# Optimization experiments

Measured on AMD Instinct MI355X. Metric: run time of the kernel, lower is better.

The kernel has to match this reference:

```python
import jax, jax.numpy as jnp
import numpy as np
import math

B, L, D, H, MAX_K = 8, 4096, 2048, 16, 1024
HD = D // H


def setup_inputs() -> dict:
    key = jax.random.key(0)
    ks = jax.random.split(key, 20)
    x = jax.random.normal(ks[0], (B, L, D), dtype=jnp.float32)
    register = jax.random.normal(ks[1], (B, D), dtype=jnp.float32)
    # mask with exactly MAX_K True per row -> max_k == MAX_K, no ragged padding
    perms = jax.vmap(lambda k: jax.random.permutation(k, L))(jax.random.split(ks[2], B))
    sel = perms[:, :MAX_K]
    mask = jnp.zeros((B, L), dtype=bool).at[jnp.arange(B)[:, None], sel].set(True)
    s = 1.0 / math.sqrt(D)
    def lin(k):
        k1, k2 = jax.random.split(k)
        return (jax.random.uniform(k1, (D, D), jnp.float32, -s, s),
                jax.random.uniform(k2, (D,), jnp.float32, -s, s))
    Wq, bq = lin(ks[3]); Wk, bk = lin(ks[4]); Wv, bv = lin(ks[5])
    Wrk, brk = lin(ks[6]); Wrv, brv = lin(ks[7]); Wo, bo = lin(ks[8])
    return {"x": x, "mask": mask, "register": register,
            "Wq": Wq, "bq": bq, "Wk": Wk, "bk": bk, "Wv": Wv, "bv": bv,
            "Wrk": Wrk, "brk": brk, "Wrv": Wrv, "brv": brv, "Wo": Wo, "bo": bo}


def reference(x, mask, register, Wq, bq, Wk, bk, Wv, bv, Wrk, brk, Wrv, brv, Wo, bo):
    Bb, Ll, Dd = x.shape
    scale = math.sqrt(HD)
    # stable argsort puts True(=selected) tokens first, in ascending position order
    idx = jnp.argsort(jnp.logical_not(mask), axis=1, stable=True)[:, :MAX_K]  # [B,K]
    pos = idx
    sig = jnp.take_along_axis(x, idx[:, :, None], axis=1)  # [B,K,D]
    Q = (sig @ Wq.T + bq).reshape(Bb, MAX_K, H, HD)
    Kt = (sig @ Wk.T + bk)
    Vt = (sig @ Wv.T + bv)
    Kr = (register @ Wrk.T + brk)[:, None, :]  # [B,1,D]
    Vr = (register @ Wrv.T + brv)[:, None, :]
    Kall = jnp.concatenate([Kt, Kr], axis=1).reshape(Bb, MAX_K + 1, H, HD)
    Vall = jnp.concatenate([Vt, Vr], axis=1).reshape(Bb, MAX_K + 1, H, HD)
    scores = jnp.einsum('bqhd,bkhd->bhqk', Q, Kall) / scale  # [B,H,K,K+1]
    causal = jnp.where(pos[:, :, None] < pos[:, None, :], -1e9, 0.0)  # [B,K,K]
    full_mask = jnp.concatenate([causal, jnp.zeros((Bb, MAX_K, 1), x.dtype)], axis=2)[:, None]
    attn = jax.nn.softmax(scores + full_mask, axis=-1)
    out = jnp.einsum('bhqk,bkhd->bqhd', attn, Vall).reshape(Bb, MAX_K, Dd)
    y = out @ Wo.T + bo
    res = x.at[jnp.arange(Bb)[:, None], idx].set(y)
    return res
```

## Files before the change

kernel.cpp:

```cpp
#include <hip/hip_runtime.h>
#include <hip/hip_bf16.h>

#define B_  8
#define L_  4096
#define D_  2048
#define H_  16
#define HD_ 128
#define MK_ 1024
#define VTP 1040

typedef __attribute__((ext_vector_type(8))) short short8;
typedef __attribute__((ext_vector_type(4))) float f32x4;

__device__ inline unsigned short f2bf(float f) {
  unsigned int u = __float_as_uint(f);
  unsigned int r = (u + 0x7fffu + ((u >> 16) & 1u)) >> 16;
  return (unsigned short)r;
}

__device__ __forceinline__ void gload_lds16(const void* g, void* l) {
  __builtin_amdgcn_global_load_lds(
      (const __attribute__((address_space(1))) void*)g,
      (__attribute__((address_space(3))) void*)l, 16, 0, 0);
}

__global__ __launch_bounds__(256) void prep1_kernel(
    const void* __restrict__ maskv, int* __restrict__ rowmap,
    const float* __restrict__ W0, const float* __restrict__ W1,
    const float* __restrict__ W2, const float* __restrict__ W3,
    unsigned short* __restrict__ Wb) {
  int bid = blockIdx.x;
  int tid = threadIdx.x;
  if (bid < 8) {
    __shared__ int cnt;
    __shared__ int cnts[256];
    const unsigned char* m8 = (const unsigned char*)maskv;
    if (tid == 0) cnt = 0;
    __syncthreads();
    int local = 0;
    for (int i = tid; i < B_ * L_; i += 256) local += (m8[i] != 0);
    atomicAdd(&cnt, local);
    __syncthreads();
    int cv = cnt;
    int t = 0;
    if (cv == B_ * MK_)      t = 0;
    else if (cv == 2 * MK_)  t = 1;
    else if (cv == 4 * MK_)  t = 2;
    int b = bid;
    unsigned char loc[16];
    int c = 0;
    for (int j = 0; j < 16; ++j) {
      int pos = tid * 16 + j;
      int mv;
      if (t == 1)      mv = ((const int*)maskv)[b * L_ + pos] != 0;
      else if (t == 2) mv = ((const float*)maskv)[b * L_ + pos] != 0.0f;
      else             mv = m8[b * L_ + pos] != 0;
      loc[j] = (unsigned char)mv; c += mv;
    }
    cnts[tid] = c;
    __syncthreads();
    for (int off = 1; off < 256; off <<= 1) {
      int v = (tid >= off) ? cnts[tid - off] : 0;
      __syncthreads();
      cnts[tid] += v;
      __syncthreads();
    }
    int rank = cnts[tid] - c;
    for (int j = 0; j < 16; ++j) {
      if (loc[j]) {
        if (rank < MK_) rowmap[b * MK_ + rank] = b * L_ + tid * 16 + j;
        ++rank;
      }
    }
  } else {
    const size_t per = (size_t)D_ * D_;
    int cb = bid - 8;
    int slab = cb >> 11;
    const float* W = (slab == 0) ? W0 : (slab == 1) ? W1 : (slab == 2) ? W2 : W3;
    size_t i = ((size_t)(cb & 2047) * 256 + tid) * 8;
    float4 a = *(const float4*)(W + i);
    float4 b4 = *(const float4*)(W + i + 4);
    uint4 o;
    o.x = f2bf(a.x)  | ((unsigned)f2bf(a.y)  << 16);
    o.y = f2bf(a.z)  | ((unsigned)f2bf(a.w)  << 16);
    o.z = f2bf(b4.x) | ((unsigned)f2bf(b4.y) << 16);
    o.w = f2bf(b4.z) | ((unsigned)f2bf(b4.w) << 16);
    *(uint4*)(Wb + slab * per + i) = o;
  }
}

__global__ __launch_bounds__(256) void prep2_kernel(
    const float* __restrict__ x, const int* __restrict__ rowmap,
    unsigned short* __restrict__ sig,
    const float* __restrict__ reg, const float* __restrict__ Wrk, const float* __restrict__ brk,
    const float* __restrict__ Wrv, const float* __restrict__ brv,
    unsigned short* __restrict__ Kb, unsigned short* __restrict__ Vt) {
  int bid = blockIdx.x;
  int tid = threadIdx.x;
  if (bid < 8192) {
    int row = bid;
    const float* src = x + (size_t)rowmap[row] * D_;
    unsigned short* dst = sig + (size_t)row * D_;
    float4 a = ((const float4*)src)[tid * 2];
    float4 b4 = ((const float4*)src)[tid * 2 + 1];
    uint4 o;
    o.x = f2bf(a.x)  | ((unsigned)f2bf(a.y)  << 16);
    o.y = f2bf(a.z)  | ((unsigned)f2bf(a.w)  << 16);
    o.z = f2bf(b4.x) | ((unsigned)f2bf(b4.y) << 16);
    o.w = f2bf(b4.z) | ((unsigned)f2bf(b4.w) << 16);
    *(uint4*)(dst + tid * 8) = o;
  } else {
    int gw = ((bid - 8192) * 256 + tid) >> 6;
    int lane = tid & 63;
    int mat = gw >> 11;
    int n = gw & 2047;
    const float* W = mat ? Wrv : Wrk;
    const float* wrow = W + (size_t)n * D_;
    float s[8] = {};
    for (int j = 0; j < 8; ++j) {
      int e = j * 256 + lane * 4;
      float4 wv = *(const float4*)(wrow + e);
#pragma unroll
      for (int b = 0; b < 8; ++b) {
        float4 rv = *(const float4*)(reg + (size_t)b * D_ + e);
        s[b] += wv.x * rv.x + wv.y * rv.y + wv.z * rv.z + wv.w * rv.w;
      }
    }
#pragma unroll
    for (int off = 32; off; off >>= 1)
#pragma unroll
      for (int b = 0; b < 8; ++b) s[b] += __shfl_down(s[b], off);
    if (lane == 0) {
      float bias = (mat ? brv : brk)[n];
#pragma unroll
      for (int b = 0; b < 8; ++b) {
        unsigned short v = f2bf(s[b] + bias);
        if (mat) {
          Vt[(((size_t)b * 16 + (n >> 7)) * 128 + (n & 127)) * VTP + 1024] = v;
        } else {
          Kb[((size_t)b * 1025 + 1024) * D_ + n] = v;
        }
      }
    }
  }
}

template<int FUSED>
__global__ __launch_bounds__(512, 2) void gemm8_kernel(
    const unsigned short* __restrict__ A, const unsigned short* __restrict__ Bw,
    const float* __restrict__ b0, const float* __restrict__ b1, const float* __restrict__ b2,
    void* __restrict__ O0, void* __restrict__ O1, void* __restrict__ O2,
    const int* __restrict__ rowmap, float qalpha, int nbt, int matfix) {
  __shared__ __align__(16) unsigned short lds[2][2][16384];
  int tid = threadIdx.x, lane = tid & 63, w = tid >> 6;
  int g = lane >> 4, l15 = lane & 15;
  int wm = w >> 2, wn = w & 3;

  int bid = blockIdx.x;
  int xcd = bid & 7, j = bid >> 3;
  int mb = xcd * 4 + j / nbt, nb = j % nbt;
  int m0 = mb * 256, n0 = nb * 256;

  f32x4 acc[2][4][4] = {};

  size_t aoff[4], boff[4];
  int ldsoff[4];
#pragma unroll
  for (int i = 0; i < 4; ++i) {
    int chunk = tid + i * 512;
    int row = chunk >> 3;
    int gslot = (chunk & 7) ^ (row & 7);
    aoff[i] = (size_t)(m0 + row) * D_ + gslot * 8;
    boff[i] = (size_t)(n0 + row) * D_ + gslot * 8;
    ldsoff[i] = (w * 64 + i * 512) * 8;
  }

#define STAGE_A(kt, BUF) {                                              \
    _Pragma("unroll")                                                   \
    for (int i_ = 0; i_ < 4; ++i_)                                      \
      gload_lds16(A + aoff[i_] + (kt) * 64, &lds[BUF][0][ldsoff[i_]]);  \
  }
#define STAGE_B(kt, BUF) {                                              \
    _Pragma("unroll")                                                   \
    for (int i_ = 0; i_ < 4; ++i_)                                      \
      gload_lds16(Bw + boff[i_] + (kt) * 64, &lds[BUF][1][ldsoff[i_]]); \
  }
#define RD_A(dst, BUF, h, kk) {                                         \
    _Pragma("unroll")                                                   \
    for (int mf_ = 0; mf_ < 4; ++mf_) {                                 \
      int r_ = wm * 128 + (h) * 64 + mf_ * 16 + l15;                    \
      dst[mf_] = *(const short8*)(&lds[BUF][0][r_ * 64 + (((kk) * 4 + g) ^ (r_ & 7)) * 8]); } \
  }
#define RD_B(dst, BUF, kk) {                                            \
    _Pragma("unroll")                                                   \
    for (int nf_ = 0; nf_ < 4; ++nf_) {                                 \
      int r_ = wn * 64 + nf_ * 16 + l15;                                \
      dst[nf_] = *(const short8*)(&lds[BUF][1][r_ * 64 + (((kk) * 4 + g) ^ (r_ & 7)) * 8]); } \
  }
#define MFMA16(h, af, bf) {                                             \
    _Pragma("unroll")                                                   \
    for (int mf_ = 0; mf_ < 4; ++mf_)                                   \
      _Pragma("unroll")                                                 \
      for (int nf_ = 0; nf_ < 4; ++nf_)                                 \
        acc[h][mf_][nf_] = __builtin_amdgcn_mfma_f32_16x16x32_bf16(af[mf_], bf[nf_], acc[h][mf_][nf_], 0, 0, 0); \
  }

  STAGE_A(0, 0); STAGE_B(0, 0);
  asm volatile("s_waitcnt vmcnt(0)" ::: "memory");
  __builtin_amdgcn_s_barrier();

  short8 afE[4], afO[4], bf0[4], bf1[4];

#define KTILE(kt, BUF)                                                    \
  {                                                                       \
    RD_B(bf0, BUF, 0); RD_B(bf1, BUF, 1); RD_A(afE, BUF, 0, 0);           \
     \
    RD_A(afO, BUF, 0, 1);                                                 \
    if ((kt) + 1 < 32) { STAGE_A((kt) + 1, BUF ^ 1); STAGE_B((kt) + 1, BUF ^ 1); } \
    asm volatile("s_waitcnt lgkmcnt(4)" ::: "memory");                    \
    __builtin_amdgcn_sched_barrier(0);                                    \
    __builtin_amdgcn_s_setprio(1);                                        \
    MFMA16(0, afE, bf0);                                                  \
    __builtin_amdgcn_s_setprio(0);                                        \
                                                       \
    RD_A(afE, BUF, 1, 0);                                                 \
    asm volatile("s_waitcnt lgkmcnt(4)" ::: "memory");                    \
    __builtin_amdgcn_sched_barrier(0);                                    \
    __builtin_amdgcn_s_setprio(1);                                        \
    MFMA16(0, afO, bf1);                                                  \
    __builtin_amdgcn_s_setprio(0);                                        \
                                                       \
    RD_A(afO, BUF, 1, 1);                                                 \
    asm volatile("s_waitcnt lgkmcnt(4)" ::: "memory");                    \
    __builtin_amdgcn_sched_barrier(0);                                    \
    __builtin_amdgcn_s_setprio(1);                                        \
    MFMA16(1, afE, bf0);                                                  \
    __builtin_amdgcn_s_setprio(0);                                        \
                                                       \
    asm volatile("s_waitcnt lgkmcnt(0)" ::: "memory");                    \
    __builtin_amdgcn_sched_barrier(0);                                    \
    __builtin_amdgcn_s_setprio(1);                                        \
    MFMA16(1, afO, bf1);                                                  \
    __builtin_amdgcn_s_setprio(0);                                        \
    asm volatile("s_waitcnt vmcnt(0)" ::: "memory");                      \
    __builtin_amdgcn_s_barrier();                                         \
  }

  for (int kt2 = 0; kt2 < 16; ++kt2) {
    KTILE(2 * kt2,     0);
    KTILE(2 * kt2 + 1, 1);
  }
#undef KTILE
#undef MFMA16
#undef RD_A
#undef RD_B
#undef STAGE_A
#undef STAGE_B

  int mat = 0;
  const float* bias = b0;
  float alpha = 1.0f;
  int n0l = n0;
  if (FUSED) {
    mat = (matfix >= 0) ? matfix : (n0 >> 11);
    bias = (mat == 0) ? b0 : ((mat == 1) ? b1 : b2);
    alpha = (mat == 0) ? qalpha : 1.0f;
    n0l = n0 & 2047;
  }

#pragma unroll
  for (int ph = 0; ph < 2; ++ph) {
#pragma unroll
    for (int mf = 0; mf < 4; ++mf) {
#pragma unroll
      for (int nf = 0; nf < 4; ++nf) {
        int nn = n0l + wn * 64 + nf * 16 + l15;
        float bvv = bias[nn];
        int m = m0 + wm * 128 + ph * 64 + mf * 16 + g * 4;
        if (FUSED) {
          if (mat == 2) {
            int bb = m >> 10, tok = m & 1023;
            size_t base = (((size_t)bb * 16 + (nn >> 7)) * 128 + (nn & 127)) * VTP + tok;
            uint2 u;
            u.x = f2bf(acc[ph][mf][nf][0] + bvv) | ((unsigned)f2bf(acc[ph][mf][nf][1] + bvv) << 16);
            u.y = f2bf(acc[ph][mf][nf][2] + bvv) | ((unsigned)f2bf(acc[ph][mf][nf][3] + bvv) << 16);
            *(uint2*)((unsigned short*)O2 + base) = u;
          } else {
            unsigned short* out = (mat == 0) ? (unsigned short*)O0 : (unsigned short*)O1;
#pragma unroll
            for (int r = 0; r < 4; ++r) {
              float v = (acc[ph][mf][nf][r] + bvv) * alpha;
              int mm = m + r;
              int row = (mat == 1) ? mm + (mm >> 10) : mm;
              out[(size_t)row * D_ + nn] = f2bf(v);
            }
          }
        } else {
#pragma unroll
          for (int r = 0; r < 4; ++r) {
            int row = rowmap[m + r];
            ((float*)O0)[(size_t)row * D_ + nn] = acc[ph][mf][nf][r] + bvv;
          }
        }
      }
    }
  }
}

__device__ __forceinline__ void stage_k(const unsigned short* Kbase, unsigned short* dst,
                                        int kv0, int w, int lane) {
#pragma unroll
  for (int i = 0; i < 2; ++i) {
    int ib = w * 2 + i;
    int row = ib * 4 + (lane >> 4);
    int sl = (lane & 15) ^ (row & 7);
    int krow = kv0 + row; if (krow > MK_) krow = MK_;
    gload_lds16(Kbase + (size_t)krow * D_ + sl * 8, dst + ib * 512);
  }
}
__device__ __forceinline__ void stage_v(const unsigned short* Vbase, unsigned short* dst,
                                        int kv0, int w, int lane) {
#pragma unroll
  for (int i = 0; i < 2; ++i) {
    int ib = w * 2 + i;
    int row = ib * 8 + (lane >> 3);
    int sl = (lane & 7) ^ (row & 7);
    gload_lds16(Vbase + (size_t)row * VTP + kv0 + sl * 8, dst + ib * 512);
  }
}

#define NF4 16777216

__global__ __launch_bounds__(512) void attn_kernel(
    const unsigned short* __restrict__ Qb, const unsigned short* __restrict__ Kb,
    const unsigned short* __restrict__ Vt, unsigned short* __restrict__ Ob,
    const float4* __restrict__ xsrc, float4* __restrict__ xdst) {
  int bx = blockIdx.x;
  int gq = bx >> 7;
  int qi = 7 - gq;
  int bh = bx & 127;
  int b = bh >> 4, h = bh & 15;
  int tid = threadIdx.x, lane = tid & 63, w = tid >> 6;
  int g = lane >> 4, l15 = lane & 15;
  int q0 = qi * 128;
  int nt = 2 * qi + 3;

  size_t cpyBase = ((size_t)128 * (18 * gq - gq * gq) + (size_t)(bx & 127) * nt) * 2048;

  __shared__ __align__(16) unsigned short Ks[64 * 128];
  __shared__ __align__(16) unsigned short Vts[128 * 64];
  __shared__ __align__(16) unsigned short Ps[8][16][72];

  const unsigned short* Kbase = Kb + (size_t)b * 1025 * D_ + h * HD_;
  const unsigned short* Vbase = Vt + (size_t)bh * 128 * VTP;

  short8 qf[4];
  {
    const unsigned short* qrow = Qb + (size_t)(b * MK_ + q0 + w * 16 + l15) * D_ + h * HD_;
#pragma unroll
    for (int kk = 0; kk < 4; ++kk) qf[kk] = *(const short8*)(qrow + kk * 32 + g * 8);
  }

  f32x4 oacc[8] = {};
  float mrow[4], lrow[4];
#pragma unroll
  for (int r = 0; r < 4; ++r) { mrow[r] = -__builtin_inff(); lrow[r] = 0.f; }

  int qminw = q0 + w * 16;

  stage_k(Kbase, Ks, 0, w, lane);

  for (int t = 0; t < nt; ++t) {
    int kv0 = (t < nt - 1) ? t * 64 : MK_;

    size_t ci[4];
    float4 cv[4];
    {
      size_t i0 = cpyBase + (size_t)t * 2048 + tid;
#pragma unroll
      for (int jj = 0; jj < 4; ++jj) {
        size_t ix = i0 + jj * 512;
        ci[jj] = ix < NF4 ? ix : (NF4 - 1);
        cv[jj] = xsrc[ci[jj]];
      }
    }

    stage_v(Vbase, Vts, kv0, w, lane);
    if (t == 0) asm volatile("s_waitcnt vmcnt(6)" ::: "memory");
    else        asm volatile("s_waitcnt vmcnt(10)" ::: "memory");
    __builtin_amdgcn_s_barrier();

    bool active = (t == nt - 1) || (t * 64 <= qminw + 15);
    f32x4 sacc[4] = {};
    if (active) {
      __builtin_amdgcn_s_setprio(1);
#pragma unroll
      for (int kk = 0; kk < 4; ++kk) {
#pragma unroll
        for (int nf = 0; nf < 4; ++nf) {
          int krow = nf * 16 + l15;
          int sw = (kk * 4 + g) ^ (krow & 7);
          short8 kf = *(const short8*)(Ks + krow * 128 + sw * 8);
          sacc[nf] = __builtin_amdgcn_mfma_f32_16x16x32_bf16(qf[kk], kf, sacc[nf], 0, 0, 0);
        }
      }
      __builtin_amdgcn_s_setprio(0);
    }

    __builtin_amdgcn_s_barrier();
    if (t + 1 < nt) {
      int kv1 = (t + 1 < nt - 1) ? (t + 1) * 64 : MK_;
      stage_k(Kbase, Ks, kv1, w, lane);
    }

    if (active) {
      if (t == nt - 1) {
#pragma unroll
        for (int nf = 0; nf < 4; ++nf) {
          int col = nf * 16 + l15;
          if (col != 0) {
#pragma unroll
            for (int r = 0; r < 4; ++r) sacc[nf][r] = -1e9f;
          }
        }
      } else if (t * 64 + 63 > qminw) {
        int qb = qminw - t * 64 + g * 4;
#pragma unroll
        for (int nf = 0; nf < 4; ++nf) {
          int col = nf * 16 + l15;
#pragma unroll
          for (int r = 0; r < 4; ++r)
            if (col > qb + r) sacc[nf][r] = -1e9f;
        }
      }

      float pm[4]; bool need = false;
#pragma unroll
      for (int r = 0; r < 4; ++r) {
        float mx = fmaxf(fmaxf(sacc[0][r], sacc[1][r]), fmaxf(sacc[2][r], sacc[3][r]));
        mx = fmaxf(mx, __shfl_xor(mx, 1));
        mx = fmaxf(mx, __shfl_xor(mx, 2));
        mx = fmaxf(mx, __shfl_xor(mx, 4));
        mx = fmaxf(mx, __shfl_xor(mx, 8));
        pm[r] = mx;
        need |= (mx > mrow[r] + 8.0f);
      }
      if (__any((int)need)) {
#pragma unroll
        for (int r = 0; r < 4; ++r) {
          float mnew = fmaxf(mrow[r], pm[r]);
          float sf = exp2f(mrow[r] - mnew);
          mrow[r] = mnew;
          lrow[r] *= sf;
#pragma unroll
          for (int i = 0; i < 8; ++i) oacc[i][r] *= sf;
        }
      }
      float rs[4] = {0.f, 0.f, 0.f, 0.f};
#pragma unroll
      for (int nf = 0; nf < 4; ++nf) {
#pragma unroll
        for (int r = 0; r < 4; ++r) {
          float p = exp2f(sacc[nf][r] - mrow[r]);
          sacc[nf][r] = p;
          rs[r] += p;
        }
      }
#pragma unroll
      for (int r = 0; r < 4; ++r) {
        float s = rs[r];
        s += __shfl_xor(s, 1);
        s += __shfl_xor(s, 2);
        s += __shfl_xor(s, 4);
        s += __shfl_xor(s, 8);
        lrow[r] += s;
      }
#pragma unroll
      for (int nf = 0; nf < 4; ++nf)
#pragma unroll
        for (int r = 0; r < 4; ++r)
          Ps[w][g * 4 + r][nf * 16 + l15] = f2bf(sacc[nf][r]);
    }

    if (t + 1 < nt) asm volatile("s_waitcnt vmcnt(2)" ::: "memory");
    else            asm volatile("s_waitcnt vmcnt(0)" ::: "memory");

#pragma unroll
    for (int jj = 0; jj < 4; ++jj) xdst[ci[jj]] = cv[jj];

    __builtin_amdgcn_s_barrier();

    if (active) {
      __builtin_amdgcn_s_setprio(1);
#pragma unroll
      for (int kk = 0; kk < 2; ++kk) {
        short8 pf = *(const short8*)(&Ps[w][l15][kk * 32 + g * 8]);
#pragma unroll
        for (int nf = 0; nf < 8; ++nf) {
          int vrow = nf * 16 + l15;
          int sw = (kk * 4 + g) ^ (vrow & 7);
          short8 vf = *(const short8*)(Vts + vrow * 64 + sw * 8);
          oacc[nf] = __builtin_amdgcn_mfma_f32_16x16x32_bf16(pf, vf, oacc[nf], 0, 0, 0);
        }
      }
      __builtin_amdgcn_s_setprio(0);
    }
    __builtin_amdgcn_s_barrier();
  }

#pragma unroll
  for (int nf = 0; nf < 8; ++nf) {
#pragma unroll
    for (int r = 0; r < 4; ++r) {
      size_t row = (size_t)b * MK_ + q0 + w * 16 + g * 4 + r;
      Ob[row * D_ + h * HD_ + nf * 16 + l15] = f2bf(oacc[nf][r] / lrow[r]);
    }
  }
}

extern "C" void kernel_launch(void* const* d_in, const int* in_sizes, int n_in,
                              void* d_out, int out_size, void* d_ws, size_t ws_size,
                              hipStream_t stream) {
  const float* x    = (const float*)d_in[0];
  const void*  mask = d_in[1];
  const float* reg  = (const float*)d_in[2];
  const float* Wq   = (const float*)d_in[3];
  const float* bq   = (const float*)d_in[4];
  const float* Wk   = (const float*)d_in[5];
  const float* bk   = (const float*)d_in[6];
  const float* Wv   = (const float*)d_in[7];
  const float* bv   = (const float*)d_in[8];
  const float* Wrk  = (const float*)d_in[9];
  const float* brk  = (const float*)d_in[10];
  const float* Wrv  = (const float*)d_in[11];
  const float* brv  = (const float*)d_in[12];
  const float* Wo   = (const float*)d_in[13];
  const float* bo   = (const float*)d_in[14];

  char* ws = (char*)d_ws;
  int* rowmap          = (int*)(ws + 256);
  char* p = ws + 66048;
  unsigned short* sig = (unsigned short*)p;              p += (size_t)8192 * 2048 * 2;
  unsigned short* Qb  = (unsigned short*)p;              p += (size_t)8192 * 2048 * 2;
  unsigned short* Kb  = (unsigned short*)p;              p += (size_t)8200 * 2048 * 2;
  unsigned short* Vtb = (unsigned short*)p;              p += ((size_t)16384 * VTP + 64) * 2;
  unsigned short* Wbf = (unsigned short*)p;
  unsigned short* Ob  = sig;

  const size_t need_fused = (size_t)(p - ws) + (size_t)8192 * 2048 * 2;
  const bool fused = (ws_size >= need_fused);

  const float qalpha = 0.08838834764831845f * 1.4426950408889634f;
  const size_t per = (size_t)2048 * 2048;

  if (fused) {
    prep1_kernel<<<8200, 256, 0, stream>>>(mask, rowmap, Wq, Wk, Wv, Wo, Wbf);
    prep2_kernel<<<9216, 256, 0, stream>>>(x, rowmap, sig, reg, Wrk, brk, Wrv, brv, Kb, Vtb);
    gemm8_kernel<1><<<768, 512, 0, stream>>>(sig, Wbf, bq, bk, bv, Qb, Kb, Vtb,
                                             nullptr, qalpha, 24, -1);
    attn_kernel<<<1024, 512, 0, stream>>>(Qb, Kb, Vtb, Ob, (const float4*)x, (float4*)d_out);
    gemm8_kernel<0><<<256, 512, 0, stream>>>(Ob, Wbf + 3 * per, bo, nullptr, nullptr,
                                             d_out, nullptr, nullptr, rowmap, 1.0f, 8, -1);
  } else {
    prep1_kernel<<<8, 256, 0, stream>>>(mask, rowmap, Wq, Wk, Wv, Wo, Wbf);
    prep2_kernel<<<9216, 256, 0, stream>>>(x, rowmap, sig, reg, Wrk, brk, Wrv, brv, Kb, Vtb);
    prep1_kernel<<<8200, 256, 0, stream>>>(mask, rowmap, Wq, Wq, Wq, Wq, Wbf);
    gemm8_kernel<1><<<256, 512, 0, stream>>>(sig, Wbf, bq, bk, bv, Qb, Kb, Vtb,
                                             nullptr, qalpha, 8, 0);
    prep1_kernel<<<8200, 256, 0, stream>>>(mask, rowmap, Wk, Wk, Wk, Wk, Wbf);
    gemm8_kernel<1><<<256, 512, 0, stream>>>(sig, Wbf, bq, bk, bv, Qb, Kb, Vtb,
                                             nullptr, qalpha, 8, 1);
    prep1_kernel<<<8200, 256, 0, stream>>>(mask, rowmap, Wv, Wv, Wv, Wv, Wbf);
    gemm8_kernel<1><<<256, 512, 0, stream>>>(sig, Wbf, bq, bk, bv, Qb, Kb, Vtb,
                                             nullptr, qalpha, 8, 2);
    attn_kernel<<<1024, 512, 0, stream>>>(Qb, Kb, Vtb, Ob, (const float4*)x, (float4*)d_out);
    prep1_kernel<<<8200, 256, 0, stream>>>(mask, rowmap, Wo, Wo, Wo, Wo, Wbf);
    gemm8_kernel<0><<<256, 512, 0, stream>>>(Ob, Wbf, bo, nullptr, nullptr,
                                             d_out, nullptr, nullptr, rowmap, 1.0f, 8, -1);
  }
}
```

Measured before the change: 513.4 us.

## Split GEMM tiles into half-tile quadrants with fine-grained staged prefetch

Restructures the 256x256 bf16 GEMM main loop so each operand tile is split into two 128-row halves, staged and consumed in four phases per k-step. Each half is prefetched into the other buffer as soon as its current copy has been read, with partial vmcnt waits and barriers between phases. This replaces one coarse wait per k-tile with finer overlap of global-to-LDS loads and MFMA work. Warp-to-output mapping changes to 64x32 subtiles per half, and the epilogue indexing is updated to match. The cost is more barriers per k-step and a more fragile wait-count schedule.

```diff
diff --git a/kernel.cpp b/kernel.cpp
--- a/kernel.cpp
+++ b/kernel.cpp
@@ -148,10 +148,10 @@
 template<int FUSED>
 __global__ __launch_bounds__(512, 2) void gemm8_kernel(
     const unsigned short* __restrict__ A, const unsigned short* __restrict__ Bw,
-    const float* __restrict__ b0, const float* __restrict__ b1, const float* __restrict__ b2,
+    const float* __restrict__ b0v, const float* __restrict__ b1v, const float* __restrict__ b2v,
     void* __restrict__ O0, void* __restrict__ O1, void* __restrict__ O2,
     const int* __restrict__ rowmap, float qalpha, int nbt, int matfix) {
-  __shared__ __align__(16) unsigned short lds[2][2][16384];
+  __shared__ __align__(16) unsigned short lds[2][2][2][8192];
   int tid = threadIdx.x, lane = tid & 63, w = tid >> 6;
   int g = lane >> 4, l15 = lane & 15;
   int wm = w >> 2, wn = w & 3;
@@ -163,133 +163,113 @@
 
   f32x4 acc[2][4][4] = {};
 
-  size_t aoff[4], boff[4];
-  int ldsoff[4];
-#pragma unroll
-  for (int i = 0; i < 4; ++i) {
-    int chunk = tid + i * 512;
-    int row = chunk >> 3;
-    int gslot = (chunk & 7) ^ (row & 7);
-    aoff[i] = (size_t)(m0 + row) * D_ + gslot * 8;
-    boff[i] = (size_t)(n0 + row) * D_ + gslot * 8;
-    ldsoff[i] = (w * 64 + i * 512) * 8;
-  }
-
-#define STAGE_A(kt, BUF) {                                              \
-    _Pragma("unroll")                                                   \
-    for (int i_ = 0; i_ < 4; ++i_)                                      \
-      gload_lds16(A + aoff[i_] + (kt) * 64, &lds[BUF][0][ldsoff[i_]]);  \
-  }
-#define STAGE_B(kt, BUF) {                                              \
-    _Pragma("unroll")                                                   \
-    for (int i_ = 0; i_ < 4; ++i_)                                      \
-      gload_lds16(Bw + boff[i_] + (kt) * 64, &lds[BUF][1][ldsoff[i_]]); \
-  }
-#define RD_A(dst, BUF, h, kk) {                                         \
-    _Pragma("unroll")                                                   \
-    for (int mf_ = 0; mf_ < 4; ++mf_) {                                 \
-      int r_ = wm * 128 + (h) * 64 + mf_ * 16 + l15;                    \
-      dst[mf_] = *(const short8*)(&lds[BUF][0][r_ * 64 + (((kk) * 4 + g) ^ (r_ & 7)) * 8]); } \
-  }
-#define RD_B(dst, BUF, kk) {                                            \
-    _Pragma("unroll")                                                   \
-    for (int nf_ = 0; nf_ < 4; ++nf_) {                                 \
-      int r_ = wn * 64 + nf_ * 16 + l15;                                \
-      dst[nf_] = *(const short8*)(&lds[BUF][1][r_ * 64 + (((kk) * 4 + g) ^ (r_ & 7)) * 8]); } \
-  }
-#define MFMA16(h, af, bf) {                                             \
-    _Pragma("unroll")                                                   \
-    for (int mf_ = 0; mf_ < 4; ++mf_)                                   \
-      _Pragma("unroll")                                                 \
-      for (int nf_ = 0; nf_ < 4; ++nf_)                                 \
-        acc[h][mf_][nf_] = __builtin_amdgcn_mfma_f32_16x16x32_bf16(af[mf_], bf[nf_], acc[h][mf_][nf_], 0, 0, 0); \
-  }
-
-  STAGE_A(0, 0); STAGE_B(0, 0);
-  asm volatile("s_waitcnt vmcnt(0)" ::: "memory");
-  __builtin_amdgcn_s_barrier();
-
-  short8 afE[4], afO[4], bf0[4], bf1[4];
-
-#define KTILE(kt, BUF)                                                    \
-  {                                                                       \
-    RD_B(bf0, BUF, 0); RD_B(bf1, BUF, 1); RD_A(afE, BUF, 0, 0);           \
-     \
-    RD_A(afO, BUF, 0, 1);                                                 \
-    if ((kt) + 1 < 32) { STAGE_A((kt) + 1, BUF ^ 1); STAGE_B((kt) + 1, BUF ^ 1); } \
-    asm volatile("s_waitcnt lgkmcnt(4)" ::: "memory");                    \
-    __builtin_amdgcn_sched_barrier(0);                                    \
-    __builtin_amdgcn_s_setprio(1);                                        \
-    MFMA16(0, afE, bf0);                                                  \
-    __builtin_amdgcn_s_setprio(0);                                        \
-                                                       \
-    RD_A(afE, BUF, 1, 0);                                                 \
-    asm volatile("s_waitcnt lgkmcnt(4)" ::: "memory");                    \
-    __builtin_amdgcn_sched_barrier(0);                                    \
-    __builtin_amdgcn_s_setprio(1);                                        \
-    MFMA16(0, afO, bf1);                                                  \
-    __builtin_amdgcn_s_setprio(0);                                        \
-                                                       \
-    RD_A(afO, BUF, 1, 1);                                                 \
-    asm volatile("s_waitcnt lgkmcnt(4)" ::: "memory");                    \
-    __builtin_amdgcn_sched_barrier(0);                                    \
-    __builtin_amdgcn_s_setprio(1);                                        \
-    MFMA16(1, afE, bf0);                                                  \
-    __builtin_amdgcn_s_setprio(0);                                        \
-                                                       \
-    asm volatile("s_waitcnt lgkmcnt(0)" ::: "memory");                    \
-    __builtin_amdgcn_sched_barrier(0);                                    \
-    __builtin_amdgcn_s_setprio(1);                                        \
-    MFMA16(1, afO, bf1);                                                  \
-    __builtin_amdgcn_s_setprio(0);                                        \
-    asm volatile("s_waitcnt vmcnt(0)" ::: "memory");                      \
-    __builtin_amdgcn_s_barrier();                                         \
-  }
-
-  for (int kt2 = 0; kt2 < 16; ++kt2) {
-    KTILE(2 * kt2,     0);
-    KTILE(2 * kt2 + 1, 1);
-  }
-#undef KTILE
-#undef MFMA16
+  int c0 = tid, c1 = tid + 512;
+  int r0 = c0 >> 3, s0 = (c0 & 7) ^ (r0 & 7);
+  int r1 = c1 >> 3, s1 = (c1 & 7) ^ (r1 & 7);
+  int dst0 = (w * 64) * 8;
+  int dst1 = (w * 64 + 512) * 8;
+
+#define STAGE(MAT, HH, BUF, kt) {                                                 \
+    const unsigned short* sp_ = (MAT) ? Bw : A;                                   \
+    int gb_ = (MAT) ? n0 : m0;                                                    \
+    gload_lds16(sp_ + (size_t)(gb_ + (HH)*128 + r0) * D_ + (kt)*64 + s0*8,        \
+                &lds[BUF][MAT][HH][dst0]);                                        \
+    gload_lds16(sp_ + (size_t)(gb_ + (HH)*128 + r1) * D_ + (kt)*64 + s1*8,        \
+                &lds[BUF][MAT][HH][dst1]);                                        \
+  }
+
+  short8 a_[4][2], bb0[2][2], bb1[2][2];
+#define RD_A(HH, BUF) { _Pragma("unroll")                                         \
+    for (int mf_ = 0; mf_ < 4; ++mf_) {                                           \
+      int rr_ = wm * 64 + mf_ * 16 + l15;                                         \
+      _Pragma("unroll")                                                           \
+      for (int ks_ = 0; ks_ < 2; ++ks_)                                           \
+        a_[mf_][ks_] = *(const short8*)(&lds[BUF][0][HH][rr_ * 64 + ((ks_*4+g)^(rr_&7))*8]); } }
+#define RD_B(DST, HH, BUF) { _Pragma("unroll")                                    \
+    for (int nf_ = 0; nf_ < 2; ++nf_) {                                           \
+      int rr_ = wn * 32 + nf_ * 16 + l15;                                         \
+      _Pragma("unroll")                                                           \
+      for (int ks_ = 0; ks_ < 2; ++ks_)                                           \
+        DST[nf_][ks_] = *(const short8*)(&lds[BUF][1][HH][rr_ * 64 + ((ks_*4+g)^(rr_&7))*8]); } }
+#define MF8(HA, NB, BSRC) { _Pragma("unroll")                                     \
+    for (int mf_ = 0; mf_ < 4; ++mf_)                                             \
+      _Pragma("unroll")                                                           \
+      for (int nf_ = 0; nf_ < 2; ++nf_)                                           \
+        _Pragma("unroll")                                                         \
+        for (int ks_ = 0; ks_ < 2; ++ks_)                                         \
+          acc[HA][mf_][(NB)+nf_] = __builtin_amdgcn_mfma_f32_16x16x32_bf16(       \
+              a_[mf_][ks_], BSRC[nf_][ks_], acc[HA][mf_][(NB)+nf_], 0, 0, 0); }
+
+  STAGE(0, 0, 0, 0); STAGE(1, 0, 0, 0); STAGE(1, 1, 0, 0); STAGE(0, 1, 0, 0);
+
+  for (int T = 0; T < 32; ++T) {
+    int BUF = T & 1;
+    bool more = (T + 1 < 32);
+    asm volatile("s_waitcnt vmcnt(4)" ::: "memory");
+    __builtin_amdgcn_s_barrier();
+    RD_A(0, BUF); RD_B(bb0, 0, BUF);
+    if (more) STAGE(0, 0, BUF ^ 1, T + 1);
+    asm volatile("s_waitcnt lgkmcnt(0)" ::: "memory");
+    __builtin_amdgcn_sched_barrier(0);
+    __builtin_amdgcn_s_setprio(1); MF8(0, 0, bb0); __builtin_amdgcn_s_setprio(0);
+    if (more) asm volatile("s_waitcnt vmcnt(4)" ::: "memory");
+    else      asm volatile("s_waitcnt vmcnt(2)" ::: "memory");
+    __builtin_amdgcn_s_barrier();
+    RD_B(bb1, 1, BUF);
+    if (more) STAGE(1, 0, BUF ^ 1, T + 1);
+    asm volatile("s_waitcnt lgkmcnt(0)" ::: "memory");
+    __builtin_amdgcn_sched_barrier(0);
+    __builtin_amdgcn_s_setprio(1); MF8(0, 2, bb1); __builtin_amdgcn_s_setprio(0);
+    if (more) asm volatile("s_waitcnt vmcnt(4)" ::: "memory");
+    else      asm volatile("s_waitcnt vmcnt(0)" ::: "memory");
+    __builtin_amdgcn_s_barrier();
+    RD_A(1, BUF);
+    if (more) STAGE(1, 1, BUF ^ 1, T + 1);
+    asm volatile("s_waitcnt lgkmcnt(0)" ::: "memory");
+    __builtin_amdgcn_sched_barrier(0);
+    __builtin_amdgcn_s_setprio(1); MF8(1, 0, bb0); __builtin_amdgcn_s_setprio(0);
+    __builtin_amdgcn_s_barrier();
+    if (more) STAGE(0, 1, BUF ^ 1, T + 1);
+    __builtin_amdgcn_s_setprio(1); MF8(1, 2, bb1); __builtin_amdgcn_s_setprio(0);
+  }
+#undef MF8
+#undef RD_B
 #undef RD_A
-#undef RD_B
-#undef STAGE_A
-#undef STAGE_B
+#undef STAGE
 
   int mat = 0;
-  const float* bias = b0;
+  const float* bias = b0v;
   float alpha = 1.0f;
   int n0l = n0;
   if (FUSED) {
     mat = (matfix >= 0) ? matfix : (n0 >> 11);
-    bias = (mat == 0) ? b0 : ((mat == 1) ? b1 : b2);
+    bias = (mat == 0) ? b0v : ((mat == 1) ? b1v : b2v);
     alpha = (mat == 0) ? qalpha : 1.0f;
     n0l = n0 & 2047;
   }
 
 #pragma unroll
-  for (int ph = 0; ph < 2; ++ph) {
+  for (int hA = 0; hA < 2; ++hA) {
 #pragma unroll
     for (int mf = 0; mf < 4; ++mf) {
 #pragma unroll
       for (int nf = 0; nf < 4; ++nf) {
-        int nn = n0l + wn * 64 + nf * 16 + l15;
+        int nn = n0l + (nf >> 1) * 128 + wn * 32 + (nf & 1) * 16 + l15;
         float bvv = bias[nn];
-        int m = m0 + wm * 128 + ph * 64 + mf * 16 + g * 4;
+        int m = m0 + hA * 128 + wm * 64 + mf * 16 + g * 4;
         if (FUSED) {
           if (mat == 2) {
             int bb = m >> 10, tok = m & 1023;
             size_t base = (((size_t)bb * 16 + (nn >> 7)) * 128 + (nn & 127)) * VTP + tok;
             uint2 u;
-            u.x = f2bf(acc[ph][mf][nf][0] + bvv) | ((unsigned)f2bf(acc[ph][mf][nf][1] + bvv) << 16);
-            u.y = f2bf(acc[ph][mf][nf][2] + bvv) | ((unsigned)f2bf(acc[ph][mf][nf][3] + bvv) << 16);
+            u.x = f2bf(acc[hA][mf][nf][0] + bvv) | ((unsigned)f2bf(acc[hA][mf][nf][1] + bvv) << 16);
+            u.y = f2bf(acc[hA][mf][nf][2] + bvv) | ((unsigned)f2bf(acc[hA][mf][nf][3] + bvv) << 16);
             *(uint2*)((unsigned short*)O2 + base) = u;
           } else {
             unsigned short* out = (mat == 0) ? (unsigned short*)O0 : (unsigned short*)O1;
 #pragma unroll
             for (int r = 0; r < 4; ++r) {
-              float v = (acc[ph][mf][nf][r] + bvv) * alpha;
+              float v = (acc[hA][mf][nf][r] + bvv) * alpha;
               int mm = m + r;
               int row = (mat == 1) ? mm + (mm >> 10) : mm;
               out[(size_t)row * D_ + nn] = f2bf(v);
@@ -299,7 +279,7 @@
 #pragma unroll
           for (int r = 0; r < 4; ++r) {
             int row = rowmap[m + r];
-            ((float*)O0)[(size_t)row * D_ + nn] = acc[ph][mf][nf][r] + bvv;
+            ((float*)O0)[(size_t)row * D_ + nn] = acc[hA][mf][nf][r] + bvv;
           }
         }
       }
```

New measurement: 503.2 us. 1.02x faster.
